# Kernel optimization log

Hardware: AMD Instinct MI355X
Metric: run time of the kernel (lower is better)

The kernel has to match this reference:

```python
import jax, jax.numpy as jnp
import numpy as np

C, H, W = 16, 128, 128   # in_features, dim0, dim1
FD, OUT, POOL = 3, 64, 2  # filter_dim, out_features, pooling
B = 32


def setup_inputs() -> dict:
    key = jax.random.key(0)
    k1, k2, k3 = jax.random.split(key, 3)
    x = jax.random.normal(k1, (B, C, H, W), dtype=jnp.float32)
    # linear_layer: weight (in*fd^2, out) scaled by 1/sqrt(in*fd^2), bias (out,)
    weight = jax.random.normal(k2, (C * FD * FD, OUT), dtype=jnp.float32) / jnp.sqrt(
        jnp.float32(C * FD * FD))
    bias = jax.random.normal(k3, (OUT,), dtype=jnp.float32)
    return {"x": x, "weight": weight, "bias": bias}


def reference(x, weight, bias):
    # The one-hot isometry tensordot + reshape is exactly im2col with patch
    # vector ordering c*FD^2 + n*FD + m, so the whole convolution() equals a
    # VALID conv with kernel[o, c, n, m] = weight[c*FD^2 + n*FD + m, o].
    kernel = weight.reshape(C, FD, FD, OUT).transpose(3, 0, 1, 2)  # OIHW
    y = jax.lax.conv_general_dilated(
        x, kernel, window_strides=(1, 1), padding='VALID',
        dimension_numbers=('NCHW', 'OIHW', 'NCHW'))  # (B, OUT, n_conv, m_conv)
    y = jax.nn.relu(y + bias[None, :, None, None])
    b, o, hc, wc = y.shape  # hc = H-FD+1 = 126
    # block max-pool POOLxPOOL (crop to multiple of POOL, as in the original)
    hp, wp = hc // POOL, wc // POOL
    y = y[:, :, :hp * POOL, :wp * POOL].reshape(b, o, hp, POOL, wp, POOL)
    y = jnp.max(y, axis=(3, 5))  # (B, OUT, hp, wp)
    return y.reshape(b, o, -1)  # (B, OUT, hp*wp)
```

## Files before the change

### kernel.cpp

```cpp
#include <hip/hip_runtime.h>


typedef __bf16 bf16x8 __attribute__((ext_vector_type(8)));
typedef float f32x16 __attribute__((ext_vector_type(16)));

#define MFMA32(A, B, C) __builtin_amdgcn_mfma_f32_32x32x16_bf16(A, B, C, 0, 0, 0)

__global__ void convert_b(const float* __restrict__ weight, char* __restrict__ ws) {
  int tau = blockIdx.x * 256 + threadIdx.x;
  if (tau >= 1152) return;
  int t = tau >> 7;
  int r = tau & 127;
  int o = r >> 1, hf = r & 1;
  __bf16 hi[8], lo[8];
#pragma unroll
  for (int j = 0; j < 8; ++j) {
    float v = weight[((hf * 8 + j) * 9 + t) * 64 + o];
    __bf16 h = (__bf16)v;
    hi[j] = h;
    lo[j] = (__bf16)(v - (float)h);
  }
  int nf = o >> 5, lo5 = o & 31;
  *(bf16x8*)(ws + (t * 2 + nf) * 1024 + (hf * 32 + lo5) * 16) = *(bf16x8*)hi;
  *(bf16x8*)(ws + 18432 + (t * 64 + o) * 32 + hf * 16) = *(bf16x8*)lo;
}

__global__ __launch_bounds__(256, 2)
void convpool_main(const float* __restrict__ x, const char* __restrict__ ws,
                   const float* __restrict__ bias, float* __restrict__ out) {
  __shared__ __align__(16) char lds[51200];
  const int tid = threadIdx.x;
  const int pr = blockIdx.x;
  const int b = blockIdx.y;
  const int r0 = 2 * pr;
  const int lane = tid & 63;
  const int wv = tid >> 6;
  const int half = lane >> 5;
  const int lo5 = lane & 31;
  const int rr = (lane >> 4) & 1;
  const int cc = lane & 15;

  bf16x8 Bh[9][2];
#pragma unroll
  for (int t = 0; t < 9; ++t)
#pragma unroll
    for (int nf = 0; nf < 2; ++nf)
      Bh[t][nf] = *(const bf16x8*)(ws + (t * 2 + nf) * 1024 + lane * 16);

#pragma unroll
  for (int k = 0; k < 5; ++k) {
    int idx = tid + 256 * k;
    if (idx < 1152)
      *(float4*)(lds + 32768 + idx * 16) =
          *(const float4*)(ws + 18432 + idx * 16);
  }

  {
    const int col = tid >> 1, hf = tid & 1;
#pragma unroll
    for (int row = 0; row < 4; ++row) {
      float v[8];
#pragma unroll
      for (int j = 0; j < 8; ++j)
        v[j] = x[((b * 16 + hf * 8 + j) * 128 + (r0 + row)) * 128 + col];
      __bf16 hi[8], lo[8];
#pragma unroll
      for (int j = 0; j < 8; ++j) {
        __bf16 h = (__bf16)v[j];
        hi[j] = h;
        lo[j] = (__bf16)(v[j] - (float)h);
      }
      const int a = row * 4096 + col * 32 + hf * 16;
      *(bf16x8*)(lds + a) = *(bf16x8*)hi;
      *(bf16x8*)(lds + 16384 + a) = *(bf16x8*)lo;
    }
  }
  __syncthreads();

  f32x16 acc[2][2];
#pragma unroll
  for (int i = 0; i < 16; ++i) {
    acc[0][0][i] = 0.f; acc[0][1][i] = 0.f;
    acc[1][0][i] = 0.f; acc[1][1][i] = 0.f;
  }

  const int colb = wv * 32 + cc;
#pragma unroll
  for (int t = 0; t < 9; ++t) {
    const int n = t / 3, m = t - 3 * n;
    const int a0 = (rr + n) * 4096 + (colb + m) * 32 + half * 16;
    const int a1 = a0 + 512;
    bf16x8 Ah0 = *(const bf16x8*)(lds + a0);
    bf16x8 Ah1 = *(const bf16x8*)(lds + a1);
    bf16x8 Al0 = *(const bf16x8*)(lds + 16384 + a0);
    bf16x8 Al1 = *(const bf16x8*)(lds + 16384 + a1);
    const int ab = 32768 + t * 2048 + lo5 * 32 + half * 16;
    bf16x8 Bl0 = *(const bf16x8*)(lds + ab);
    bf16x8 Bl1 = *(const bf16x8*)(lds + ab + 1024);
    acc[0][0] = MFMA32(Ah0, Bh[t][0], acc[0][0]);
    acc[1][0] = MFMA32(Ah1, Bh[t][0], acc[1][0]);
    acc[0][1] = MFMA32(Ah0, Bh[t][1], acc[0][1]);
    acc[1][1] = MFMA32(Ah1, Bh[t][1], acc[1][1]);
    acc[0][0] = MFMA32(Al0, Bh[t][0], acc[0][0]);
    acc[1][0] = MFMA32(Al1, Bh[t][0], acc[1][0]);
    acc[0][1] = MFMA32(Al0, Bh[t][1], acc[0][1]);
    acc[1][1] = MFMA32(Al1, Bh[t][1], acc[1][1]);
    acc[0][0] = MFMA32(Ah0, Bl0, acc[0][0]);
    acc[1][0] = MFMA32(Ah1, Bl0, acc[1][0]);
    acc[0][1] = MFMA32(Ah0, Bl1, acc[0][1]);
    acc[1][1] = MFMA32(Ah1, Bl1, acc[1][1]);
  }

  __syncthreads();
  float* ps = (float*)lds;
  const float bv0 = bias[lo5];
  const float bv1 = bias[32 + lo5];
#pragma unroll
  for (int mt = 0; mt < 2; ++mt) {
#pragma unroll
    for (int nf = 0; nf < 2; ++nf) {
      const f32x16 a = acc[mt][nf];
      const int o = nf * 32 + lo5;
      const float bvv = nf ? bv1 : bv0;
#pragma unroll
      for (int g = 0; g < 4; ++g) {
        float mx = fmaxf(fmaxf(a[2 * g], a[2 * g + 1]),
                         fmaxf(a[8 + 2 * g], a[9 + 2 * g]));
        float v = fmaxf(mx + bvv, 0.0f);
        int pcc = 2 * half + (g & 1) + 4 * (g >> 1);
        int pc = (wv * 2 + mt) * 8 + pcc;
        ps[o * 65 + pc] = v;
      }
    }
  }
  __syncthreads();
  {
    int o = tid >> 2, seg = tid & 3;
    int ob = ((b * 64 + o) * 63 + pr) * 63;
#pragma unroll
    for (int k2 = 0; k2 < 16; ++k2) {
      int pc = seg * 16 + k2;
      if (pc < 63) out[ob + pc] = ps[o * 65 + pc];
    }
  }
}

extern "C" void kernel_launch(void* const* d_in, const int* in_sizes, int n_in,
                              void* d_out, int out_size, void* d_ws, size_t ws_size,
                              hipStream_t stream) {
  const float* x = (const float*)d_in[0];
  const float* wgt = (const float*)d_in[1];
  const float* bias = (const float*)d_in[2];
  float* out = (float*)d_out;
  char* ws = (char*)d_ws;
  convert_b<<<dim3(5), 256, 0, stream>>>(wgt, ws);
  convpool_main<<<dim3(63, 32), 256, 0, stream>>>(x, ws, bias, out);
}
```

Baseline: 43.06 us.

## Process four pooled rows per block with rolling LDS row buffer

Each block now computes up to four pooled output rows instead of one. Input rows sit in a 4-row circular LDS buffer, so adjacent pooled rows reuse the overlapping conv input rows rather than reloading and reconverting them. The low-part weights are held in registers instead of LDS, and the grid shrinks from 63x32 to 16x32 blocks. In exchange there are fewer blocks for the GPU's CUs, more register pressure from keeping both weight halves resident, and a serial loop with per-iteration barriers.

Measured after the change: 37.99 us. 11.8% less time.

```diff
diff --git a/kernel.cpp b/kernel.cpp
--- a/kernel.cpp
+++ b/kernel.cpp
@@ -21,127 +21,137 @@
     lo[j] = (__bf16)(v - (float)h);
   }
   int nf = o >> 5, lo5 = o & 31;
-  *(bf16x8*)(ws + (t * 2 + nf) * 1024 + (hf * 32 + lo5) * 16) = *(bf16x8*)hi;
-  *(bf16x8*)(ws + 18432 + (t * 64 + o) * 32 + hf * 16) = *(bf16x8*)lo;
+  int off = (t * 2 + nf) * 1024 + (hf * 32 + lo5) * 16;
+  *(bf16x8*)(ws + off) = *(bf16x8*)hi;
+  *(bf16x8*)(ws + 18432 + off) = *(bf16x8*)lo;
+}
+
+__device__ __forceinline__ void stage_row(char* lds, const float* xb, int r,
+                                          int colS, int hfS) {
+  float v[8];
+#pragma unroll
+  for (int j = 0; j < 8; ++j) v[j] = xb[j * 16384 + r * 128];
+  __bf16 hi[8], lo[8];
+#pragma unroll
+  for (int j = 0; j < 8; ++j) {
+    __bf16 h = (__bf16)v[j];
+    hi[j] = h;
+    lo[j] = (__bf16)(v[j] - (float)h);
+  }
+  int a = ((r & 3) << 13) + hfS * 2048 + colS * 16;
+  *(bf16x8*)(lds + a) = *(bf16x8*)hi;
+  *(bf16x8*)(lds + a + 4096) = *(bf16x8*)lo;
 }
 
 __global__ __launch_bounds__(256, 2)
 void convpool_main(const float* __restrict__ x, const char* __restrict__ ws,
                    const float* __restrict__ bias, float* __restrict__ out) {
-  __shared__ __align__(16) char lds[51200];
+  __shared__ __align__(16) char lds[48896];
   const int tid = threadIdx.x;
-  const int pr = blockIdx.x;
+  const int s = blockIdx.x;
   const int b = blockIdx.y;
-  const int r0 = 2 * pr;
+  const int nr = min(4, 63 - 4 * s);
+  const int rb = 8 * s;
   const int lane = tid & 63;
   const int wv = tid >> 6;
   const int half = lane >> 5;
   const int lo5 = lane & 31;
   const int rr = (lane >> 4) & 1;
   const int cc = lane & 15;
+  const int colS = tid >> 1;
+  const int hfS = tid & 1;
+  const float* xb = x + (b * 16 + hfS * 8) * 16384 + colS;
 
-  bf16x8 Bh[9][2];
+  bf16x8 Bh[9][2], Bl[9][2];
 #pragma unroll
   for (int t = 0; t < 9; ++t)
 #pragma unroll
-    for (int nf = 0; nf < 2; ++nf)
-      Bh[t][nf] = *(const bf16x8*)(ws + (t * 2 + nf) * 1024 + lane * 16);
+    for (int nf = 0; nf < 2; ++nf) {
+      int off = (t * 2 + nf) * 1024 + lane * 16;
+      Bh[t][nf] = *(const bf16x8*)(ws + off);
+      Bl[t][nf] = *(const bf16x8*)(ws + 18432 + off);
+    }
 
 #pragma unroll
-  for (int k = 0; k < 5; ++k) {
-    int idx = tid + 256 * k;
-    if (idx < 1152)
-      *(float4*)(lds + 32768 + idx * 16) =
-          *(const float4*)(ws + 18432 + idx * 16);
-  }
-
-  {
-    const int col = tid >> 1, hf = tid & 1;
-#pragma unroll
-    for (int row = 0; row < 4; ++row) {
-      float v[8];
-#pragma unroll
-      for (int j = 0; j < 8; ++j)
-        v[j] = x[((b * 16 + hf * 8 + j) * 128 + (r0 + row)) * 128 + col];
-      __bf16 hi[8], lo[8];
-#pragma unroll
-      for (int j = 0; j < 8; ++j) {
-        __bf16 h = (__bf16)v[j];
-        hi[j] = h;
-        lo[j] = (__bf16)(v[j] - (float)h);
-      }
-      const int a = row * 4096 + col * 32 + hf * 16;
-      *(bf16x8*)(lds + a) = *(bf16x8*)hi;
-      *(bf16x8*)(lds + 16384 + a) = *(bf16x8*)lo;
-    }
-  }
+  for (int r = 0; r < 4; ++r) stage_row(lds, xb, rb + r, colS, hfS);
   __syncthreads();
 
-  f32x16 acc[2][2];
-#pragma unroll
-  for (int i = 0; i < 16; ++i) {
-    acc[0][0][i] = 0.f; acc[0][1][i] = 0.f;
-    acc[1][0][i] = 0.f; acc[1][1][i] = 0.f;
-  }
-
-  const int colb = wv * 32 + cc;
-#pragma unroll
-  for (int t = 0; t < 9; ++t) {
-    const int n = t / 3, m = t - 3 * n;
-    const int a0 = (rr + n) * 4096 + (colb + m) * 32 + half * 16;
-    const int a1 = a0 + 512;
-    bf16x8 Ah0 = *(const bf16x8*)(lds + a0);
-    bf16x8 Ah1 = *(const bf16x8*)(lds + a1);
-    bf16x8 Al0 = *(const bf16x8*)(lds + 16384 + a0);
-    bf16x8 Al1 = *(const bf16x8*)(lds + 16384 + a1);
-    const int ab = 32768 + t * 2048 + lo5 * 32 + half * 16;
-    bf16x8 Bl0 = *(const bf16x8*)(lds + ab);
-    bf16x8 Bl1 = *(const bf16x8*)(lds + ab + 1024);
-    acc[0][0] = MFMA32(Ah0, Bh[t][0], acc[0][0]);
-    acc[1][0] = MFMA32(Ah1, Bh[t][0], acc[1][0]);
-    acc[0][1] = MFMA32(Ah0, Bh[t][1], acc[0][1]);
-    acc[1][1] = MFMA32(Ah1, Bh[t][1], acc[1][1]);
-    acc[0][0] = MFMA32(Al0, Bh[t][0], acc[0][0]);
-    acc[1][0] = MFMA32(Al1, Bh[t][0], acc[1][0]);
-    acc[0][1] = MFMA32(Al0, Bh[t][1], acc[0][1]);
-    acc[1][1] = MFMA32(Al1, Bh[t][1], acc[1][1]);
-    acc[0][0] = MFMA32(Ah0, Bl0, acc[0][0]);
-    acc[1][0] = MFMA32(Ah1, Bl0, acc[1][0]);
-    acc[0][1] = MFMA32(Ah0, Bl1, acc[0][1]);
-    acc[1][1] = MFMA32(Ah1, Bl1, acc[1][1]);
-  }
-
-  __syncthreads();
-  float* ps = (float*)lds;
+  float* ps = (float*)(lds + 32768);
   const float bv0 = bias[lo5];
   const float bv1 = bias[32 + lo5];
+  const int colb16 = half * 2048 + (wv * 32 + cc) * 16;
+
+  for (int i = 0; i < nr; ++i) {
+    const int pr = 4 * s + i;
+    const int i2 = 2 * i;
+
+    f32x16 acc[2][2];
 #pragma unroll
-  for (int mt = 0; mt < 2; ++mt) {
+    for (int q = 0; q < 16; ++q) {
+      acc[0][0][q] = 0.f; acc[0][1][q] = 0.f;
+      acc[1][0][q] = 0.f; acc[1][1][q] = 0.f;
+    }
+
 #pragma unroll
-    for (int nf = 0; nf < 2; ++nf) {
-      const f32x16 a = acc[mt][nf];
-      const int o = nf * 32 + lo5;
-      const float bvv = nf ? bv1 : bv0;
+    for (int t = 0; t < 9; ++t) {
+      const int n = t / 3, m = t - 3 * n;
+      const int sb = ((i2 + rr + n) & 3) << 13;
+      const int a0 = sb + colb16 + m * 16;
+      const int a1 = a0 + 256;
+      bf16x8 Ah0 = *(const bf16x8*)(lds + a0);
+      bf16x8 Ah1 = *(const bf16x8*)(lds + a1);
+      bf16x8 Al0 = *(const bf16x8*)(lds + a0 + 4096);
+      bf16x8 Al1 = *(const bf16x8*)(lds + a1 + 4096);
+      acc[0][0] = MFMA32(Ah0, Bh[t][0], acc[0][0]);
+      acc[1][0] = MFMA32(Ah1, Bh[t][0], acc[1][0]);
+      acc[0][1] = MFMA32(Ah0, Bh[t][1], acc[0][1]);
+      acc[1][1] = MFMA32(Ah1, Bh[t][1], acc[1][1]);
+      acc[0][0] = MFMA32(Al0, Bh[t][0], acc[0][0]);
+      acc[1][0] = MFMA32(Al1, Bh[t][0], acc[1][0]);
+      acc[0][1] = MFMA32(Al0, Bh[t][1], acc[0][1]);
+      acc[1][1] = MFMA32(Al1, Bh[t][1], acc[1][1]);
+      acc[0][0] = MFMA32(Ah0, Bl[t][0], acc[0][0]);
+      acc[1][0] = MFMA32(Ah1, Bl[t][0], acc[1][0]);
+      acc[0][1] = MFMA32(Ah0, Bl[t][1], acc[0][1]);
+      acc[1][1] = MFMA32(Ah1, Bl[t][1], acc[1][1]);
+    }
+
 #pragma unroll
-      for (int g = 0; g < 4; ++g) {
-        float mx = fmaxf(fmaxf(a[2 * g], a[2 * g + 1]),
-                         fmaxf(a[8 + 2 * g], a[9 + 2 * g]));
-        float v = fmaxf(mx + bvv, 0.0f);
-        int pcc = 2 * half + (g & 1) + 4 * (g >> 1);
-        int pc = (wv * 2 + mt) * 8 + pcc;
-        ps[o * 65 + pc] = v;
+    for (int mt = 0; mt < 2; ++mt)
+#pragma unroll
+      for (int nf = 0; nf < 2; ++nf) {
+        const f32x16 a = acc[mt][nf];
+        const int o = nf * 32 + lo5;
+        const float bvv = nf ? bv1 : bv0;
+#pragma unroll
+        for (int g = 0; g < 4; ++g) {
+          float mx = fmaxf(fmaxf(a[2 * g], a[2 * g + 1]),
+                           fmaxf(a[8 + 2 * g], a[9 + 2 * g]));
+          float v = fmaxf(mx + bvv, 0.0f);
+          int pcc = 2 * half + (g & 1) + 4 * (g >> 1);
+          int pc = (wv * 2 + mt) * 8 + pcc;
+          if (pc < 63) ps[o * 63 + pc] = v;
+        }
+      }
+    __syncthreads();
+
+    if (i < nr - 1) {
+      stage_row(lds, xb, rb + i2 + 4, colS, hfS);
+      stage_row(lds, xb, rb + i2 + 5, colS, hfS);
+    }
+    {
+      const int ob = ((b * 64) * 63 + pr) * 63;
+#pragma unroll
+      for (int v = 0; v < 16; ++v) {
+        int idx = tid + 256 * v;
+        if (idx < 4032) {
+          int o = idx / 63;
+          int pc = idx - o * 63;
+          out[ob + o * 3969 + pc] = ps[idx];
+        }
       }
     }
-  }
-  __syncthreads();
-  {
-    int o = tid >> 2, seg = tid & 3;
-    int ob = ((b * 64 + o) * 63 + pr) * 63;
-#pragma unroll
-    for (int k2 = 0; k2 < 16; ++k2) {
-      int pc = seg * 16 + k2;
-      if (pc < 63) out[ob + pc] = ps[o * 65 + pc];
-    }
+    __syncthreads();
   }
 }
 
@@ -154,5 +164,5 @@
   float* out = (float*)d_out;
   char* ws = (char*)d_ws;
   convert_b<<<dim3(5), 256, 0, stream>>>(wgt, ws);
-  convpool_main<<<dim3(63, 32), 256, 0, stream>>>(x, ws, bias, out);
+  convpool_main<<<dim3(16, 32), 256, 0, stream>>>(x, ws, bias, out);
 }
```
